# Performance work log

Hardware: AMD Instinct MI355X
Metric: run time of the kernel (lower is better)

## Reference

```python
import jax, jax.numpy as jnp
import numpy as np
from jax import lax

NH = 8          # heads
DK = 64         # total key/query depth
DV = 64         # total value depth
DKH = DK // NH  # per-head key depth = 8
DVH = DV // NH  # per-head value depth = 8
H = W = 32
CIN = 256
FILTERS = 256


def rel_to_abs(x):
    # x: [B, N, L, 2L-1] relative logits -> [B, N, L, L] absolute logits
    B, N, L, _ = x.shape
    x = jnp.pad(x, ((0, 0), (0, 0), (0, 0), (0, 1)))          # [B,N,L,2L]
    flat = x.reshape(B, N, L * 2 * L)
    flat = jnp.pad(flat, ((0, 0), (0, 0), (0, L - 1)))        # [B,N,2L^2+L-1]
    final = flat.reshape(B, N, L + 1, 2 * L - 1)
    return final[:, :, :L, L - 1:]


def rel_logits_1d(q, rel_k, h, w, perm):
    # q: [B, NH, h, w, DKH], rel_k: [2w-1, DKH]
    B = q.shape[0]
    rel = jnp.einsum('bnxyd,md->bnxym', q, rel_k)             # [B,NH,h,w,2w-1]
    rel = rel.reshape(B, NH * h, w, 2 * w - 1)
    rel = rel_to_abs(rel)                                     # [B,NH*h,w,w]
    rel = rel.reshape(B, NH, h, w, w)[:, :, :, None]          # [B,NH,h,1,w,w]
    rel = jnp.broadcast_to(rel, (B, NH, h, h, w, w))          # tile over other axis
    rel = jnp.transpose(rel, perm)
    return rel.reshape(B, NH, h * w, h * w)


def setup_inputs() -> dict:
    key = jax.random.key(0)
    ks = jax.random.split(key, 6)
    s = lambda fan_in: 1.0 / np.sqrt(fan_in)
    return {
        'x': jax.random.normal(ks[0], (8, H, W, CIN), jnp.float32),
        'conv_w': jax.random.normal(ks[1], (3, 3, CIN, FILTERS - DV), jnp.float32) * s(9 * CIN),
        'conv_b': jnp.zeros((FILTERS - DV,), jnp.float32),
        'qkv_w': jax.random.normal(ks[2], (CIN, 2 * DK + DV), jnp.float32) * s(CIN),
        'qkv_b': jnp.zeros((2 * DK + DV,), jnp.float32),
        'attn_w': jax.random.normal(ks[3], (DV, DV), jnp.float32) * s(DV),
        'attn_b': jnp.zeros((DV,), jnp.float32),
        'key_rel_w': jax.random.normal(ks[4], (2 * W - 1, DKH), jnp.float32),
        'key_rel_h': jax.random.normal(ks[5], (2 * H - 1, DKH), jnp.float32),
    }


def reference(x, conv_w, conv_b, qkv_w, qkv_b, attn_w, attn_b, key_rel_w, key_rel_h):
    B = x.shape[0]
    # standard conv branch (SAME padding)
    conv_out = lax.conv_general_dilated(
        x, conv_w, window_strides=(1, 1), padding='SAME',
        dimension_numbers=('NHWC', 'HWIO', 'NHWC')) + conv_b

    # 1x1 qkv projection
    kqv = jnp.einsum('bhwc,co->bhwo', x, qkv_w) + qkv_b
    k = kqv[..., :DK]
    q = kqv[..., DK:2 * DK] * (DKH ** -0.5)
    v = kqv[..., 2 * DK:]

    def split_heads(t, d):
        return t.reshape(B, H, W, NH, d).transpose(0, 3, 1, 2, 4)  # [B,NH,H,W,d]

    qh = split_heads(q, DKH)
    kh = split_heads(k, DKH)
    vh = split_heads(v, DVH)

    qf = qh.reshape(B, NH, H * W, DKH)
    kf = kh.reshape(B, NH, H * W, DKH)
    vf = vh.reshape(B, NH, H * W, DVH)

    logits = jnp.einsum('bnid,bnjd->bnij', qf, kf)            # [B,NH,HW,HW]
    rel_w = rel_logits_1d(qh, key_rel_w, H, W, (0, 1, 2, 4, 3, 5))
    qh_t = qh.transpose(0, 1, 3, 2, 4)                        # [B,NH,W,H,d]
    rel_h = rel_logits_1d(qh_t, key_rel_h, W, H, (0, 1, 4, 2, 5, 3))
    logits = logits + rel_w + rel_h

    weights = jax.nn.softmax(logits, axis=-1)
    attn = jnp.einsum('bnij,bnjd->bnid', weights, vf)         # [B,NH,HW,DVH]
    attn = attn.reshape(B, NH, H, W, DVH).transpose(0, 2, 3, 1, 4).reshape(B, H, W, DV)
    attn = jnp.einsum('bhwc,co->bhwo', attn, attn_w) + attn_b

    return jnp.concatenate([conv_out, attn], axis=3)
```

## Files before the change

kernel.cpp:

```cpp
#include <hip/hip_runtime.h>
#include <cstdint>

using u16 = unsigned short;
using u32 = uint32_t;

typedef __attribute__((ext_vector_type(8))) short bf16x8;
typedef __attribute__((ext_vector_type(4))) float f32x4;

__device__ __forceinline__ float bf2f(u16 v) { return __uint_as_float(((u32)v) << 16); }
__device__ __forceinline__ u16 f2bf(float f) {
    u32 u = __float_as_uint(f);
    u += 0x7fffu + ((u >> 16) & 1u);
    return (u16)(u >> 16);
}
__device__ __forceinline__ u16 bf16u(float f) {
#if defined(__BF16_MANT_DIG__)
    __bf16 h = (__bf16)f;
    return __builtin_bit_cast(u16, h);
#else
    return f2bf(f);
#endif
}
__device__ __forceinline__ float fexp2(float x) {
#if __has_builtin(__builtin_amdgcn_exp2f)
    return __builtin_amdgcn_exp2f(x);
#else
    float r; asm("v_exp_f32 %0, %1" : "=v"(r) : "v"(x)); return r;
#endif
}

__device__ __forceinline__ int block_flag(const u16* __restrict__ x) {
    __shared__ int cnt;
    if (threadIdx.x == 0) cnt = 0;
    __syncthreads();
    int c = 0;
    #pragma unroll
    for (int k = 0; k < 16; k++) {
        u16 v = x[threadIdx.x * 16 + k];
        int e = (v >> 7) & 0xFF;
        c += (e >= 110 && e <= 140) ? 1 : 0;
    }
    atomicAdd(&cnt, c);
    __syncthreads();
    return (cnt > 3300) ? 1 : 0;
}

#define FLAG_OFF 0
#define ZERO_OFF 8
#define WSH_OFF  2097168
#define AWF_OFF  2588688
#define CBF_OFF  2592784
#define QBF_OFF  2592976
#define ABF_OFF  2593168
#define KRW_OFF  2593232
#define KRH_OFF  2593736
#define KB_OFF   2594240
#define QB_OFF   3118528
#define VB_OFF   3642816
#define AT_OFF   4167104
#define XBF_OFF  4691392
#define WSHQ_OFF 9409984

__global__ __launch_bounds__(256) void prepx_kernel(
    const u16* __restrict__ x0,
    const void* __restrict__ cw, const void* __restrict__ qw,
    const void* __restrict__ cb, const void* __restrict__ qb,
    const void* __restrict__ aw, const void* __restrict__ ab,
    const void* __restrict__ kw_, const void* __restrict__ kh_,
    u16* __restrict__ wshC, u16* __restrict__ wshQ,
    float* __restrict__ cbf, float* __restrict__ qbf, float* __restrict__ awf,
    float* __restrict__ abf, float* __restrict__ krw, float* __restrict__ krh,
    float* __restrict__ zbuf, int* __restrict__ flagws, u16* __restrict__ xbf)
{
    const int blk = blockIdx.x;
    const int fl = block_flag(x0);
    if (blk == 0 && threadIdx.x == 0) *flagws = fl;

    if (blk < 240) {
        const void* w; u16* o; int g;
        if (blk < 216) { w = cw; o = wshC; g = blk * 256 + threadIdx.x; }
        else           { w = qw; o = wshQ; g = (blk - 216) * 256 + threadIdx.x; }
        const int kk = g / 768, rem = g % 768;
        const int tile = rem >> 6, lane = rem & 63;
        const int n = tile * 16 + (lane & 15);
        u16 tmp[8];
        #pragma unroll
        for (int j = 0; j < 8; j++) {
            const size_t k = (size_t)(kk * 32 + ((lane >> 4) << 3) + j);
            tmp[j] = fl ? ((const u16*)w)[k * 192 + n]
                        : f2bf(((const float*)w)[k * 192 + n]);
        }
        *(uint4*)(o + (size_t)g * 8) = *(const uint4*)tmp;
    } else if (blk < 262) {
        const int gid = (blk - 240) * 256 + threadIdx.x;
        const void* src; float* dst; int e;
        if      (gid <  192) { src = cb;  dst = cbf; e = gid; }
        else if (gid <  384) { src = qb;  dst = qbf; e = gid - 192; }
        else if (gid < 4480) { src = aw;  dst = awf; e = gid - 384; }
        else if (gid < 4544) { src = ab;  dst = abf; e = gid - 4480; }
        else if (gid < 5048) { src = kw_; dst = krw; e = gid - 4544; }
        else if (gid < 5552) { src = kh_; dst = krh; e = gid - 5048; }
        else if (gid < 5568) { zbuf[gid - 5552] = 0.f; return; }
        else return;
        dst[e] = fl ? bf2f(((const u16*)src)[e]) : ((const float*)src)[e];
    } else {
        const int g = (blk - 262) * 256 + threadIdx.x;
        if (fl) {
            *(uint4*)(xbf + (size_t)g * 8) = *(const uint4*)(x0 + (size_t)g * 8);
        } else {
            const float* src = (const float*)x0 + (size_t)g * 8;
            float4 a = *(const float4*)src, b = *(const float4*)(src + 4);
            uint4 o;
            o.x = (u32)f2bf(a.x) | ((u32)f2bf(a.y) << 16);
            o.y = (u32)f2bf(a.z) | ((u32)f2bf(a.w) << 16);
            o.z = (u32)f2bf(b.x) | ((u32)f2bf(b.y) << 16);
            o.w = (u32)f2bf(b.z) | ((u32)f2bf(b.w) << 16);
            *(uint4*)(xbf + (size_t)g * 8) = o;
        }
    }
}

__global__ __launch_bounds__(256) void qc_kernel(
    const u16* __restrict__ xbf, const u16* __restrict__ wshC, const u16* __restrict__ wshQ,
    const float* __restrict__ cbf, const float* __restrict__ qbf_,
    const int* __restrict__ flagws,
    u16* __restrict__ kb16, float* __restrict__ qbuf, u16* __restrict__ vb16,
    void* __restrict__ out)
{
    __shared__ u16 xs[3 * 34 * 264];
    const int blk = blockIdx.x;
    const int t = threadIdx.x;
    const int lane = t & 63, wave = t >> 6;
    const int Mtile = wave & 1;
    const int l15 = lane & 15, quad = lane >> 4;

    if (blk < 512) {
        const int coh = blk & 1, row = blk >> 1;
        const int b = row >> 5, h = row & 31;
        const int fl = *flagws;

        #pragma unroll
        for (int r = 0; r < 3; ++r) {
            const int hh = h + r - 1;
            if (t < 64) {
                const int s = (t >> 5) ? 33 : 0, cq = t & 31;
                *(uint4*)(xs + (r * 34 + s) * 264 + cq * 8) = make_uint4(0, 0, 0, 0);
            }
            const bool ok = (hh >= 0) && (hh < 32);
            const u16* src = xbf + ((size_t)((b * 32 + (ok ? hh : 0)) * 32)) * 256;
            #pragma unroll
            for (int i = 0; i < 4; ++i) {
                const int idx = t + i * 256;
                const int px = idx >> 5, cq = idx & 31;
                uint4 v = ok ? *(const uint4*)(src + px * 256 + cq * 8)
                             : make_uint4(0, 0, 0, 0);
                *(uint4*)(xs + (r * 34 + 1 + px) * 264 + cq * 8) = v;
            }
        }
        __syncthreads();

        const int tg0 = coh * 6 + (wave >> 1) * 3;
        f32x4 acc[3] = {{0,0,0,0},{0,0,0,0},{0,0,0,0}};

        #pragma unroll
        for (int p = 0; p < 9; ++p) {
            const int kh = p / 3, kw = p - kh * 3;
            const u16* ap = xs + (kh * 34 + kw + Mtile * 16 + l15) * 264 + quad * 8;
            #pragma unroll
            for (int ck = 0; ck < 8; ++ck) {
                const int kk = p * 8 + ck;
                const bf16x8 av = *(const bf16x8*)(ap + ck * 32);
                const u16* wp = wshC + ((size_t)(kk * 12 + tg0) * 64 + lane) * 8;
                const bf16x8 b0 = *(const bf16x8*)(wp);
                const bf16x8 b1 = *(const bf16x8*)(wp + 512);
                const bf16x8 b2 = *(const bf16x8*)(wp + 1024);
                acc[0] = __builtin_amdgcn_mfma_f32_16x16x32_bf16(av, b0, acc[0], 0, 0, 0);
                acc[1] = __builtin_amdgcn_mfma_f32_16x16x32_bf16(av, b1, acc[1], 0, 0, 0);
                acc[2] = __builtin_amdgcn_mfma_f32_16x16x32_bf16(av, b2, acc[2], 0, 0, 0);
            }
        }

        const int px0 = Mtile * 16 + quad * 4;
        #pragma unroll
        for (int ti = 0; ti < 3; ++ti) {
            const int co = (tg0 + ti) * 16 + l15;
            const float bias = cbf[co];
            #pragma unroll
            for (int r = 0; r < 4; ++r) {
                const size_t oidx = ((size_t)row * 32 + px0 + r) * 256 + co;
                const float v = acc[ti][r] + bias;
                if (fl) ((u16*)out)[oidx] = f2bf(v);
                else    ((float*)out)[oidx] = v;
            }
        }
    } else {
        const int idx2 = blk - 512;
        const int coh = idx2 & 1, row = idx2 >> 1;
        const int b = row >> 5, h = row & 31;

        {
            const u16* src = xbf + (size_t)row * 8192;
            #pragma unroll
            for (int i = 0; i < 4; ++i) {
                const int idx = t + i * 256;
                const int px = idx >> 5, cq = idx & 31;
                *(uint4*)(xs + px * 264 + cq * 8) = *(const uint4*)(src + px * 256 + cq * 8);
            }
        }
        __syncthreads();

        const int tg0 = coh * 6 + (wave >> 1) * 3;
        f32x4 acc[3] = {{0,0,0,0},{0,0,0,0},{0,0,0,0}};

        const u16* ap = xs + (Mtile * 16 + l15) * 264 + quad * 8;
        #pragma unroll
        for (int kk = 0; kk < 8; ++kk) {
            const bf16x8 av = *(const bf16x8*)(ap + kk * 32);
            const u16* wp = wshQ + ((size_t)(kk * 12 + tg0) * 64 + lane) * 8;
            const bf16x8 b0 = *(const bf16x8*)(wp);
            const bf16x8 b1 = *(const bf16x8*)(wp + 512);
            const bf16x8 b2 = *(const bf16x8*)(wp + 1024);
            acc[0] = __builtin_amdgcn_mfma_f32_16x16x32_bf16(av, b0, acc[0], 0, 0, 0);
            acc[1] = __builtin_amdgcn_mfma_f32_16x16x32_bf16(av, b1, acc[1], 0, 0, 0);
            acc[2] = __builtin_amdgcn_mfma_f32_16x16x32_bf16(av, b2, acc[2], 0, 0, 0);
        }

        const int px0 = Mtile * 16 + quad * 4;
        #pragma unroll
        for (int ti = 0; ti < 3; ++ti) {
            const int tg = tg0 + ti;
            const int o = tg * 16 + l15;
            const int third = tg >> 2;
            const int within = o - third * 64;
            const int n = within >> 3, d = within & 7;
            const float bias = qbf_[o];
            #pragma unroll
            for (int r = 0; r < 4; ++r) {
                const int i = h * 32 + px0 + r;
                const size_t off = ((size_t)(b * 8 + n) * 1024 + i) * 8 + d;
                const float val = acc[ti][r] + bias;
                if (third == 0)      kb16[off] = f2bf(val);
                else if (third == 1) qbuf[off] = val * 0.51006973050f;
                else                 vb16[off] = f2bf(val);
            }
        }
    }
}

#define ATTN_STEPA(C, KA, KB, OACC)                                            \
  do {                                                                         \
    const int c_ = (C);                                                        \
    const float rhv = sRH[c_ * 36 + pair * 16 + l15];                          \
    f32x4 acc0, acc1;                                                          \
    acc0[0] = rhv + rw0[0]; acc0[1] = rhv + rw0[1];                            \
    acc0[2] = rhv + rw0[2]; acc0[3] = rhv + rw0[3];                            \
    acc1[0] = rhv + rw1[0]; acc1[1] = rhv + rw1[1];                            \
    acc1[2] = rhv + rw1[2]; acc1[3] = rhv + rw1[3];                            \
    acc0 = __builtin_amdgcn_mfma_f32_16x16x32_bf16(KA, Aq.v, acc0, 0, 0, 0);   \
    acc1 = __builtin_amdgcn_mfma_f32_16x16x32_bf16(KB, Aq.v, acc1, 0, 0, 0);   \
    if (c_ + 4 < 32) {                \
      KA = *(const bf16x8*)(kp0 + (c_ + 4) * 256);                             \
      KB = *(const bf16x8*)(kp1 + (c_ + 4) * 256);                             \
    }                                                                          \
    union { u16 a[8]; bf16x8 v; } pf;                                          \
    pf.a[0] = bf16u(fexp2(fminf(acc0[0], 80.0f)));                             \
    pf.a[1] = bf16u(fexp2(fminf(acc0[1], 80.0f)));                             \
    pf.a[2] = bf16u(fexp2(fminf(acc0[2], 80.0f)));                             \
    pf.a[3] = bf16u(fexp2(fminf(acc0[3], 80.0f)));                             \
    pf.a[4] = bf16u(fexp2(fminf(acc1[0], 80.0f)));                             \
    pf.a[5] = bf16u(fexp2(fminf(acc1[1], 80.0f)));                             \
    pf.a[6] = bf16u(fexp2(fminf(acc1[2], 80.0f)));                             \
    pf.a[7] = bf16u(fexp2(fminf(acc1[3], 80.0f)));                             \
    bf16x8 Av;                                                                 \
    if (l15 < 8) Av = *(const bf16x8*)(sVT + l15 * 1032 + c_ * 32 + quad * 8); \
    else         Av = ONE.v;                                                   \
    OACC = __builtin_amdgcn_mfma_f32_16x16x32_bf16(Av, pf.v, OACC, 0, 0, 0);   \
  } while (0)

__global__ __launch_bounds__(256) void attn_mfma_kernel(
    const u16* __restrict__ kb16, const float* __restrict__ qbuf, const u16* __restrict__ vb16,
    const float* __restrict__ krw, const float* __restrict__ krh,
    float* __restrict__ attnbuf)
{
    const int qb = blockIdx.x;
    const int bn = blockIdx.y;
    const int b = bn >> 3, hn = bn & 7;
    const int t = threadIdx.x;
    const int i0 = qb * 32;

    __shared__ __align__(16) u16   sVT[8 * 1032];
    __shared__ __align__(16) u16   sRW[32 * 40];
    __shared__ __align__(16) float sRH[32 * 36];
    __shared__ __align__(16) float sRed[2 * 64 * 4];

    const u16* vg = vb16 + (size_t)bn * 8192;
    #pragma unroll
    for (int k4 = 0; k4 < 4; k4++) {
        const int key = t + k4 * 256;
        uint4 vv = *(const uint4*)(vg + key * 8);
        sVT[0 * 1032 + key] = (u16)(vv.x);  sVT[1 * 1032 + key] = (u16)(vv.x >> 16);
        sVT[2 * 1032 + key] = (u16)(vv.y);  sVT[3 * 1032 + key] = (u16)(vv.y >> 16);
        sVT[4 * 1032 + key] = (u16)(vv.z);  sVT[5 * 1032 + key] = (u16)(vv.z >> 16);
        sVT[6 * 1032 + key] = (u16)(vv.w);  sVT[7 * 1032 + key] = (u16)(vv.w >> 16);
    }
    #pragma unroll
    for (int k8 = 0; k8 < 4; k8++) {
        const int idx = t + k8 * 256;
        const int il = idx >> 5, w = idx & 31;
        const int i = i0 + il;
        const float* q = qbuf + ((size_t)bn * 1024 + i) * 8;
        float4 qa = *(const float4*)q, qc = *(const float4*)(q + 4);
        const float* rp = krw + (size_t)(w - (i & 31) + 31) * 8;
        float4 ra = *(const float4*)rp, rc = *(const float4*)(rp + 4);
        sRW[il * 40 + w] = f2bf(qa.x*ra.x + qa.y*ra.y + qa.z*ra.z + qa.w*ra.w
                              + qc.x*rc.x + qc.y*rc.y + qc.z*rc.z + qc.w*rc.w);
        const float* hp = krh + (size_t)(w - (i >> 5) + 31) * 8;
        float4 ha = *(const float4*)hp, hc = *(const float4*)(hp + 4);
        sRH[w * 36 + il] = qa.x*ha.x + qa.y*ha.y + qa.z*ha.z + qa.w*ha.w
                         + qc.x*hc.x + qc.y*hc.y + qc.z*hc.z + qc.w*hc.w;
    }
    __syncthreads();

    const int lane = t & 63, wave = t >> 6;
    const int pair = wave >> 1, sub = wave & 1;
    const int l15 = lane & 15, quad = lane >> 4;

    union Frag { u16 a[8]; bf16x8 v; };
    Frag Aq;
    {
        const float* q = qbuf + ((size_t)bn * 1024 + i0 + pair * 16 + l15) * 8;
        float4 qa = *(const float4*)q, qc = *(const float4*)(q + 4);
        Aq.a[0] = f2bf(qa.x); Aq.a[1] = f2bf(qa.y); Aq.a[2] = f2bf(qa.z); Aq.a[3] = f2bf(qa.w);
        Aq.a[4] = f2bf(qc.x); Aq.a[5] = f2bf(qc.y); Aq.a[6] = f2bf(qc.z); Aq.a[7] = f2bf(qc.w);
        if (quad != 0) {
            #pragma unroll
            for (int j = 0; j < 8; j++) Aq.a[j] = 0;
        }
    }
    const bf16x8 Arw = *(const bf16x8*)(sRW + (pair * 16 + l15) * 40 + quad * 8);

    Frag S0, S1, ONE;
    #pragma unroll
    for (int j = 0; j < 8; j++) { S0.a[j] = 0; S1.a[j] = 0; ONE.a[j] = 0x3F80; }
    if (quad == (l15 >> 2)) {
        S0.a[l15 & 3]       = 0x3F80;
        S1.a[4 + (l15 & 3)] = 0x3F80;
    }

    f32x4 zero4 = {0.f, 0.f, 0.f, 0.f};
    const f32x4 rw0 = __builtin_amdgcn_mfma_f32_16x16x32_bf16(S0.v, Arw, zero4, 0, 0, 0);
    const f32x4 rw1 = __builtin_amdgcn_mfma_f32_16x16x32_bf16(S1.v, Arw, zero4, 0, 0, 0);

    const u16* kg = kb16 + (size_t)bn * 8192;
    const int s = l15 >> 2, rr = l15 & 3;
    const u16* kp0 = kg + (size_t)(8 * s + rr) * 8;
    const u16* kp1 = kg + (size_t)(8 * s + 4 + rr) * 8;

    f32x4 oaccE = {0.f, 0.f, 0.f, 0.f};
    f32x4 oaccO = {0.f, 0.f, 0.f, 0.f};

    bf16x8 kAa = *(const bf16x8*)(kp0 + sub * 256);
    bf16x8 kBa = *(const bf16x8*)(kp1 + sub * 256);
    bf16x8 kAb = *(const bf16x8*)(kp0 + (sub + 2) * 256);
    bf16x8 kBb = *(const bf16x8*)(kp1 + (sub + 2) * 256);

    for (int c2 = sub; c2 < 32; c2 += 4) {
        ATTN_STEPA(c2,     kAa, kBa, oaccE);
        ATTN_STEPA(c2 + 2, kAb, kBb, oaccO);
    }

    f32x4 oacc;
    oacc[0] = oaccE[0] + oaccO[0];
    oacc[1] = oaccE[1] + oaccO[1];
    oacc[2] = oaccE[2] + oaccO[2];
    oacc[3] = oaccE[3] + oaccO[3];

    if (sub == 1) *(f32x4*)(sRed + (pair * 64 + lane) * 4) = oacc;
    __syncthreads();
    if (sub == 0) {
        const f32x4 part = *(const f32x4*)(sRed + (pair * 64 + lane) * 4);
        oacc[0] += part[0]; oacc[1] += part[1];
        oacc[2] += part[2]; oacc[3] += part[3];

        const float lr = __shfl(oacc[0], 32 + l15, 64);
        const float inv = 1.0f / fmaxf(lr, 1e-30f);
        if (quad < 2) {
            float4 o;
            o.x = oacc[0] * inv; o.y = oacc[1] * inv;
            o.z = oacc[2] * inv; o.w = oacc[3] * inv;
            *(float4*)(attnbuf + ((size_t)b * 1024 + i0 + pair * 16 + l15) * 64
                       + hn * 8 + quad * 4) = o;
        }
    }
}

__global__ __launch_bounds__(256) void proj_kernel(
    const float* __restrict__ attnbuf, const float* __restrict__ awf, const float* __restrict__ abf,
    const int* __restrict__ flagws, void* __restrict__ out)
{
    const int g = blockIdx.x * 256 + threadIdx.x;
    const int px = g >> 6, o = g & 63;
    const float* ar = attnbuf + (size_t)px * 64;
    float acc = abf[o];
    #pragma unroll 8
    for (int c = 0; c < 64; c++) acc += ar[c] * awf[c * 64 + o];
    if (*flagws) ((u16*)out)[(size_t)px * 256 + 192 + o] = f2bf(acc);
    else         ((float*)out)[(size_t)px * 256 + 192 + o] = acc;
}

extern "C" void kernel_launch(void* const* d_in, const int* in_sizes, int n_in,
                              void* d_out, int out_size, void* d_ws, size_t ws_size,
                              hipStream_t stream)
{
    float* ws = (float*)d_ws;
    int*   flag = (int*)(ws + FLAG_OFF);
    float* zbuf = ws + ZERO_OFF;
    u16*   wsh  = (u16*)(ws + WSH_OFF);
    float* awf  = ws + AWF_OFF;
    float* cbf  = ws + CBF_OFF;
    float* qbf  = ws + QBF_OFF;
    float* abf  = ws + ABF_OFF;
    float* krw  = ws + KRW_OFF;
    float* krh  = ws + KRH_OFF;
    u16*   kb16 = (u16*)(ws + KB_OFF);
    float* qbuf = ws + QB_OFF;
    u16*   vb16 = (u16*)(ws + VB_OFF);
    float* atb  = ws + AT_OFF;
    u16*   xbf  = (u16*)(ws + XBF_OFF);
    u16*   wshQ = (u16*)(ws + WSHQ_OFF);

    prepx_kernel<<<1286, 256, 0, stream>>>(
        (const u16*)d_in[0],
        d_in[1], d_in[3], d_in[2], d_in[4], d_in[5], d_in[6], d_in[7], d_in[8],
        wsh, wshQ, cbf, qbf, awf, abf, krw, krh, zbuf, flag, xbf);

    qc_kernel<<<1024, 256, 0, stream>>>(
        xbf, wsh, wshQ, cbf, qbf, flag, kb16, qbuf, vb16, d_out);

    attn_mfma_kernel<<<dim3(32, 64), 256, 0, stream>>>(kb16, qbuf, vb16, krw, krh, atb);
    proj_kernel     <<<2048,         256, 0, stream>>>(atb, awf, abf, flag, d_out);
}
```

Before: 147.2 us.

## Pre-pad input in global memory and read conv/QKV operands directly instead of via LDS

The prep kernel now writes the bf16 input into a zero-padded 34x34 spatial layout, with extra blocks zeroing the border. The conv and QKV GEMM paths then load A operands straight from global memory (relying on cache), dropping the shared-memory staging, the border-zeroing logic and the __syncthreads barrier. This removes LDS traffic and the barrier and should raise occupancy, since the large shared array is gone. In exchange, each A fragment is fetched repeatedly from L1/L2 across the nine taps, and the padded buffer uses slightly more workspace.

```diff
diff --git a/kernel.cpp b/kernel.cpp
--- a/kernel.cpp
+++ b/kernel.cpp
@@ -70,9 +70,22 @@
     u16* __restrict__ wshC, u16* __restrict__ wshQ,
     float* __restrict__ cbf, float* __restrict__ qbf, float* __restrict__ awf,
     float* __restrict__ abf, float* __restrict__ krw, float* __restrict__ krh,
-    float* __restrict__ zbuf, int* __restrict__ flagws, u16* __restrict__ xbf)
+    float* __restrict__ zbuf, int* __restrict__ flagws, u16* __restrict__ xp)
 {
     const int blk = blockIdx.x;
+    if (blk >= 1286) {
+        const int z = (blk - 1286) * 256 + threadIdx.x;
+        const int b = z / 4224, r = z % 4224;
+        const int p = r >> 5, cu = r & 31;
+        int hh, ww;
+        if      (p < 34)  { hh = 0;        ww = p; }
+        else if (p < 68)  { hh = 33;       ww = p - 34; }
+        else if (p < 100) { hh = p - 67;   ww = 0; }
+        else              { hh = p - 99;   ww = 33; }
+        *(uint4*)(xp + (((size_t)(b * 34 + hh) * 34) + ww) * 256 + cu * 8)
+            = make_uint4(0, 0, 0, 0);
+        return;
+    }
     const int fl = block_flag(x0);
     if (blk == 0 && threadIdx.x == 0) *flagws = fl;
 
@@ -105,29 +118,32 @@
         dst[e] = fl ? bf2f(((const u16*)src)[e]) : ((const float*)src)[e];
     } else {
         const int g = (blk - 262) * 256 + threadIdx.x;
+        const int b = g >> 15, r = g & 32767;
+        const int h = r >> 10, r2 = r & 1023;
+        const int w = r2 >> 5, cu = r2 & 31;
+        u16* dst = xp + (((size_t)(b * 34 + h + 1) * 34) + w + 1) * 256 + cu * 8;
         if (fl) {
-            *(uint4*)(xbf + (size_t)g * 8) = *(const uint4*)(x0 + (size_t)g * 8);
+            *(uint4*)dst = *(const uint4*)(x0 + (size_t)g * 8);
         } else {
             const float* src = (const float*)x0 + (size_t)g * 8;
-            float4 a = *(const float4*)src, b = *(const float4*)(src + 4);
+            float4 a = *(const float4*)src, c4 = *(const float4*)(src + 4);
             uint4 o;
-            o.x = (u32)f2bf(a.x) | ((u32)f2bf(a.y) << 16);
-            o.y = (u32)f2bf(a.z) | ((u32)f2bf(a.w) << 16);
-            o.z = (u32)f2bf(b.x) | ((u32)f2bf(b.y) << 16);
-            o.w = (u32)f2bf(b.z) | ((u32)f2bf(b.w) << 16);
-            *(uint4*)(xbf + (size_t)g * 8) = o;
+            o.x = (u32)f2bf(a.x)  | ((u32)f2bf(a.y)  << 16);
+            o.y = (u32)f2bf(a.z)  | ((u32)f2bf(a.w)  << 16);
+            o.z = (u32)f2bf(c4.x) | ((u32)f2bf(c4.y) << 16);
+            o.w = (u32)f2bf(c4.z) | ((u32)f2bf(c4.w) << 16);
+            *(uint4*)dst = o;
         }
     }
 }
 
 __global__ __launch_bounds__(256) void qc_kernel(
-    const u16* __restrict__ xbf, const u16* __restrict__ wshC, const u16* __restrict__ wshQ,
+    const u16* __restrict__ xp, const u16* __restrict__ wshC, const u16* __restrict__ wshQ,
     const float* __restrict__ cbf, const float* __restrict__ qbf_,
     const int* __restrict__ flagws,
     u16* __restrict__ kb16, float* __restrict__ qbuf, u16* __restrict__ vb16,
     void* __restrict__ out)
 {
-    __shared__ u16 xs[3 * 34 * 264];
     const int blk = blockIdx.x;
     const int t = threadIdx.x;
     const int lane = t & 63, wave = t >> 6;
@@ -138,34 +154,14 @@
         const int coh = blk & 1, row = blk >> 1;
         const int b = row >> 5, h = row & 31;
         const int fl = *flagws;
-
-        #pragma unroll
-        for (int r = 0; r < 3; ++r) {
-            const int hh = h + r - 1;
-            if (t < 64) {
-                const int s = (t >> 5) ? 33 : 0, cq = t & 31;
-                *(uint4*)(xs + (r * 34 + s) * 264 + cq * 8) = make_uint4(0, 0, 0, 0);
-            }
-            const bool ok = (hh >= 0) && (hh < 32);
-            const u16* src = xbf + ((size_t)((b * 32 + (ok ? hh : 0)) * 32)) * 256;
-            #pragma unroll
-            for (int i = 0; i < 4; ++i) {
-                const int idx = t + i * 256;
-                const int px = idx >> 5, cq = idx & 31;
-                uint4 v = ok ? *(const uint4*)(src + px * 256 + cq * 8)
-                             : make_uint4(0, 0, 0, 0);
-                *(uint4*)(xs + (r * 34 + 1 + px) * 264 + cq * 8) = v;
-            }
-        }
-        __syncthreads();
-
         const int tg0 = coh * 6 + (wave >> 1) * 3;
         f32x4 acc[3] = {{0,0,0,0},{0,0,0,0},{0,0,0,0}};
 
+        const u16* xb = xp + ((size_t)(b * 34 + h) * 34 + Mtile * 16 + l15) * 256 + quad * 8;
         #pragma unroll
         for (int p = 0; p < 9; ++p) {
             const int kh = p / 3, kw = p - kh * 3;
-            const u16* ap = xs + (kh * 34 + kw + Mtile * 16 + l15) * 264 + quad * 8;
+            const u16* ap = xb + (size_t)(kh * 34 + kw) * 256;
             #pragma unroll
             for (int ck = 0; ck < 8; ++ck) {
                 const int kk = p * 8 + ck;
@@ -197,22 +193,11 @@
         const int idx2 = blk - 512;
         const int coh = idx2 & 1, row = idx2 >> 1;
         const int b = row >> 5, h = row & 31;
-
-        {
-            const u16* src = xbf + (size_t)row * 8192;
-            #pragma unroll
-            for (int i = 0; i < 4; ++i) {
-                const int idx = t + i * 256;
-                const int px = idx >> 5, cq = idx & 31;
-                *(uint4*)(xs + px * 264 + cq * 8) = *(const uint4*)(src + px * 256 + cq * 8);
-            }
-        }
-        __syncthreads();
-
         const int tg0 = coh * 6 + (wave >> 1) * 3;
         f32x4 acc[3] = {{0,0,0,0},{0,0,0,0},{0,0,0,0}};
 
-        const u16* ap = xs + (Mtile * 16 + l15) * 264 + quad * 8;
+        const u16* ap = xp + (((size_t)(b * 34 + h + 1) * 34) + 1 + Mtile * 16 + l15) * 256
+                        + quad * 8;
         #pragma unroll
         for (int kk = 0; kk < 8; ++kk) {
             const bf16x8 av = *(const bf16x8*)(ap + kk * 32);
@@ -426,16 +411,16 @@
     float* qbuf = ws + QB_OFF;
     u16*   vb16 = (u16*)(ws + VB_OFF);
     float* atb  = ws + AT_OFF;
-    u16*   xbf  = (u16*)(ws + XBF_OFF);
+    u16*   xp   = (u16*)(ws + XBF_OFF);
     u16*   wshQ = (u16*)(ws + WSHQ_OFF);
 
-    prepx_kernel<<<1286, 256, 0, stream>>>(
+    prepx_kernel<<<1418, 256, 0, stream>>>(
         (const u16*)d_in[0],
         d_in[1], d_in[3], d_in[2], d_in[4], d_in[5], d_in[6], d_in[7], d_in[8],
-        wsh, wshQ, cbf, qbf, awf, abf, krw, krh, zbuf, flag, xbf);
+        wsh, wshQ, cbf, qbf, awf, abf, krw, krh, zbuf, flag, xp);
 
     qc_kernel<<<1024, 256, 0, stream>>>(
-        xbf, wsh, wshQ, cbf, qbf, flag, kb16, qbuf, vb16, d_out);
+        xp, wsh, wshQ, cbf, qbf, flag, kb16, qbuf, vb16, d_out);
 
     attn_mfma_kernel<<<dim3(32, 64), 256, 0, stream>>>(kb16, qbuf, vb16, krw, krh, atb);
     proj_kernel     <<<2048,         256, 0, stream>>>(atb, awf, abf, flag, d_out);
```

Measured after the change: 156.0 us. 6.0% more time.

## Double-buffer conv input rows in LDS to shrink shared memory and overlap staging

Applied to the files above, without the earlier changes.

The conv branch used to stage all three input rows into LDS before computing. It now uses a two-slot buffer: it loads rows 0 and 1, computes kernel row 0, then loads row 2 into slot 0 while computing kernel row 1, and finally computes kernel row 2. The LDS footprint drops from three rows to two, which should allow more resident blocks and hides part of the global load latency behind MFMA work. The cost is two extra barriers. The other branch also uses xs, so it must fit within the smaller array.

```diff
diff --git a/kernel.cpp b/kernel.cpp
--- a/kernel.cpp
+++ b/kernel.cpp
@@ -127,7 +127,7 @@
     u16* __restrict__ kb16, float* __restrict__ qbuf, u16* __restrict__ vb16,
     void* __restrict__ out)
 {
-    __shared__ u16 xs[3 * 34 * 264];
+    __shared__ u16 xs[2 * 34 * 264];
     const int blk = blockIdx.x;
     const int t = threadIdx.x;
     const int lane = t & 63, wave = t >> 6;
@@ -138,47 +138,57 @@
         const int coh = blk & 1, row = blk >> 1;
         const int b = row >> 5, h = row & 31;
         const int fl = *flagws;
-
-        #pragma unroll
-        for (int r = 0; r < 3; ++r) {
-            const int hh = h + r - 1;
-            if (t < 64) {
-                const int s = (t >> 5) ? 33 : 0, cq = t & 31;
-                *(uint4*)(xs + (r * 34 + s) * 264 + cq * 8) = make_uint4(0, 0, 0, 0);
-            }
-            const bool ok = (hh >= 0) && (hh < 32);
-            const u16* src = xbf + ((size_t)((b * 32 + (ok ? hh : 0)) * 32)) * 256;
-            #pragma unroll
-            for (int i = 0; i < 4; ++i) {
-                const int idx = t + i * 256;
-                const int px = idx >> 5, cq = idx & 31;
-                uint4 v = ok ? *(const uint4*)(src + px * 256 + cq * 8)
-                             : make_uint4(0, 0, 0, 0);
-                *(uint4*)(xs + (r * 34 + 1 + px) * 264 + cq * 8) = v;
-            }
-        }
-        __syncthreads();
-
         const int tg0 = coh * 6 + (wave >> 1) * 3;
         f32x4 acc[3] = {{0,0,0,0},{0,0,0,0},{0,0,0,0}};
 
-        #pragma unroll
-        for (int p = 0; p < 9; ++p) {
-            const int kh = p / 3, kw = p - kh * 3;
-            const u16* ap = xs + (kh * 34 + kw + Mtile * 16 + l15) * 264 + quad * 8;
-            #pragma unroll
-            for (int ck = 0; ck < 8; ++ck) {
-                const int kk = p * 8 + ck;
-                const bf16x8 av = *(const bf16x8*)(ap + ck * 32);
-                const u16* wp = wshC + ((size_t)(kk * 12 + tg0) * 64 + lane) * 8;
-                const bf16x8 b0 = *(const bf16x8*)(wp);
-                const bf16x8 b1 = *(const bf16x8*)(wp + 512);
-                const bf16x8 b2 = *(const bf16x8*)(wp + 1024);
-                acc[0] = __builtin_amdgcn_mfma_f32_16x16x32_bf16(av, b0, acc[0], 0, 0, 0);
-                acc[1] = __builtin_amdgcn_mfma_f32_16x16x32_bf16(av, b1, acc[1], 0, 0, 0);
-                acc[2] = __builtin_amdgcn_mfma_f32_16x16x32_bf16(av, b2, acc[2], 0, 0, 0);
-            }
-        }
+        #define STAGE_ROW(R, S)                                                  \
+          do {                                                                   \
+            const int hh = h + (R) - 1;                                          \
+            if (t < 64) {                                                        \
+                const int e = (t >> 5) ? 33 : 0, cq = t & 31;                    \
+                *(uint4*)(xs + ((S) * 34 + e) * 264 + cq * 8) = make_uint4(0,0,0,0); \
+            }                                                                    \
+            const bool ok = (hh >= 0) && (hh < 32);                              \
+            const u16* src = xbf + ((size_t)((b * 32 + (ok ? hh : 0)) * 32)) * 256; \
+            _Pragma("unroll")                                                    \
+            for (int i = 0; i < 4; ++i) {                                        \
+                const int idx = t + i * 256;                                     \
+                const int px = idx >> 5, cq = idx & 31;                          \
+                uint4 v = ok ? *(const uint4*)(src + px * 256 + cq * 8)          \
+                             : make_uint4(0, 0, 0, 0);                           \
+                *(uint4*)(xs + ((S) * 34 + 1 + px) * 264 + cq * 8) = v;          \
+            }                                                                    \
+          } while (0)
+
+        #define CONV_KH(KH, S)                                                   \
+          do {                                                                   \
+            _Pragma("unroll")                                                    \
+            for (int kw = 0; kw < 3; ++kw) {                                     \
+              const u16* ap = xs + ((S) * 34 + kw + Mtile * 16 + l15) * 264 + quad * 8; \
+              _Pragma("unroll")                                                  \
+              for (int ck = 0; ck < 8; ++ck) {                                   \
+                const int kk = ((KH) * 3 + kw) * 8 + ck;                         \
+                const bf16x8 av = *(const bf16x8*)(ap + ck * 32);                \
+                const u16* wp = wshC + ((size_t)(kk * 12 + tg0) * 64 + lane) * 8;\
+                const bf16x8 b0 = *(const bf16x8*)(wp);                          \
+                const bf16x8 b1 = *(const bf16x8*)(wp + 512);                    \
+                const bf16x8 b2 = *(const bf16x8*)(wp + 1024);                   \
+                acc[0] = __builtin_amdgcn_mfma_f32_16x16x32_bf16(av, b0, acc[0], 0, 0, 0); \
+                acc[1] = __builtin_amdgcn_mfma_f32_16x16x32_bf16(av, b1, acc[1], 0, 0, 0); \
+                acc[2] = __builtin_amdgcn_mfma_f32_16x16x32_bf16(av, b2, acc[2], 0, 0, 0); \
+              }                                                                  \
+            }                                                                    \
+          } while (0)
+
+        STAGE_ROW(0, 0);
+        STAGE_ROW(1, 1);
+        __syncthreads();
+        CONV_KH(0, 0);
+        __syncthreads();
+        STAGE_ROW(2, 0);
+        CONV_KH(1, 1);
+        __syncthreads();
+        CONV_KH(2, 0);
 
         const int px0 = Mtile * 16 + quad * 4;
         #pragma unroll
@@ -193,6 +203,8 @@
                 else    ((float*)out)[oidx] = v;
             }
         }
+        #undef STAGE_ROW
+        #undef CONV_KH
     } else {
         const int idx2 = blk - 512;
         const int coh = idx2 & 1, row = idx2 >> 1;
```

After: 145.3 us. Within noise of the previous version (-1.3%).
